# Kernel optimization log

Hardware: AMD Instinct MI355X
Metric: run time of the kernel (lower is better)

Reference implementation:

```python
import jax, jax.numpy as jnp
import numpy as np

FP8_MAX = 448.0   # e4m3 max finite value
BLOCK = 128


def _cast_e4m3(v):
    """Fake-cast to fp8 e4m3: round to nearest representable value (3 mantissa bits,
    min normal exponent -6, subnormal step 2^-9), saturate at +-448."""
    a = jnp.minimum(jnp.abs(v), FP8_MAX)
    e = jnp.floor(jnp.log2(jnp.maximum(a, jnp.float32(2.0) ** -9)))
    e = jnp.maximum(e, -6.0)                 # subnormal range
    step = jnp.exp2(e - 3.0)                 # 3 mantissa bits
    q = jnp.round(a / step) * step
    q = jnp.minimum(q, FP8_MAX)
    return jnp.sign(v) * q


def fake_quant_blockwise(x, br, bc):
    """Per-(br x bc)-tile scale = amax/448, cast to e4m3, dequantize."""
    R, C = x.shape
    xt = x.reshape(R // br, br, C // bc, bc)
    amax = jnp.max(jnp.abs(xt), axis=(1, 3), keepdims=True)
    scale = jnp.maximum(amax, 1e-12) / FP8_MAX
    q = _cast_e4m3(xt / scale) * scale
    return q.reshape(R, C)


def setup_inputs() -> dict:
    key = jax.random.key(0)
    k1, k2 = jax.random.split(key)
    x = jax.random.normal(k1, (8192, 4096), dtype=jnp.float32)
    weight = jax.random.normal(k2, (4096, 4096), dtype=jnp.float32) * 0.02
    bias = jnp.zeros((4096,), dtype=jnp.float32)
    return {"x": x, "weight": weight, "bias": bias}


def reference(x, weight, bias):
    # activations: per-row 1x128 blocks (is_left); weight: 128x128 square tiles (is_sqtile)
    x_fq = fake_quant_blockwise(x, 1, BLOCK)
    w_fq = fake_quant_blockwise(weight, BLOCK, BLOCK)
    return jnp.einsum('ti,oi->to', x_fq, w_fq) + bias
```

## Files before the change

kernel.cpp:

```cpp
#include <hip/hip_runtime.h>

#define M_DIM 8192
#define N_DIM 4096
#define K_DIM 4096

typedef __bf16 bf16x8 __attribute__((ext_vector_type(8)));
typedef float f32x4 __attribute__((ext_vector_type(4)));

__device__ __forceinline__ unsigned short f2bf(float f) {
    unsigned u = __float_as_uint(f);
    u += 0x7FFFu + ((u >> 16) & 1u);
    return (unsigned short)(u >> 16);
}

__device__ __forceinline__ float cast_e4m3(float v) {
    float a = fminf(fabsf(v), 448.0f);
    float am = fmaxf(a, 0x1p-9f);
    int e = (int)((__float_as_uint(am) >> 23) & 0xFFu) - 127;
    e = (e < -6) ? -6 : e;
    float step = __uint_as_float((unsigned)(e - 3 + 127) << 23);
    float q = rintf(a / step) * step;
    q = fminf(q, 448.0f);
    return (v < 0.0f) ? -q : q;
}

__global__ __launch_bounds__(256) void quant_x(const float* __restrict__ X,
                                               unsigned short* __restrict__ Xq) {
    const int g = threadIdx.x >> 5;
    const int l = threadIdx.x & 31;
    const long rb = (long)blockIdx.x * 8 + g;
    const int row = (int)(rb >> 5);
    const int kb = (int)(rb & 31);
    const size_t base = (size_t)row * K_DIM + kb * 128 + l * 4;
    const float4 v = *(const float4*)&X[base];
    float amax = fmaxf(fmaxf(fabsf(v.x), fabsf(v.y)), fmaxf(fabsf(v.z), fabsf(v.w)));
    #pragma unroll
    for (int m = 16; m >= 1; m >>= 1)
        amax = fmaxf(amax, __shfl_xor(amax, m));
    const float scale = fmaxf(amax, 1e-12f) / 448.0f;
    ushort4 o;
    o.x = f2bf(cast_e4m3(v.x / scale) * scale);
    o.y = f2bf(cast_e4m3(v.y / scale) * scale);
    o.z = f2bf(cast_e4m3(v.z / scale) * scale);
    o.w = f2bf(cast_e4m3(v.w / scale) * scale);
    *(ushort4*)&Xq[base] = o;
}

__global__ __launch_bounds__(256) void quant_w(const float* __restrict__ W,
                                               unsigned short* __restrict__ Wq) {
    const int tile = blockIdx.x;
    const int tr = tile >> 5;
    const int tc = tile & 31;
    const int t = threadIdx.x;
    const int c4 = (t & 31) * 4;
    const float* base = W + (size_t)(tr * 128) * K_DIM + tc * 128;

    float4 v[16];
    float amax = 0.0f;
    #pragma unroll
    for (int p = 0; p < 16; ++p) {
        const int r = p * 8 + (t >> 5);
        v[p] = *(const float4*)&base[(size_t)r * K_DIM + c4];
        amax = fmaxf(amax, fmaxf(fmaxf(fabsf(v[p].x), fabsf(v[p].y)),
                                 fmaxf(fabsf(v[p].z), fabsf(v[p].w))));
    }
    #pragma unroll
    for (int m = 32; m >= 1; m >>= 1)
        amax = fmaxf(amax, __shfl_xor(amax, m));
    __shared__ float red[4];
    if ((t & 63) == 0) red[t >> 6] = amax;
    __syncthreads();
    const float am4 = fmaxf(fmaxf(red[0], red[1]), fmaxf(red[2], red[3]));
    const float scale = fmaxf(am4, 1e-12f) / 448.0f;

    unsigned short* out = Wq + (size_t)(tr * 128) * K_DIM + tc * 128;
    #pragma unroll
    for (int p = 0; p < 16; ++p) {
        const int r = p * 8 + (t >> 5);
        ushort4 o;
        o.x = f2bf(cast_e4m3(v[p].x / scale) * scale);
        o.y = f2bf(cast_e4m3(v[p].y / scale) * scale);
        o.z = f2bf(cast_e4m3(v[p].z / scale) * scale);
        o.w = f2bf(cast_e4m3(v[p].w / scale) * scale);
        *(ushort4*)&out[(size_t)r * K_DIM + c4] = o;
    }
}

#define GLOAD16(g, l)                                                          \
    __builtin_amdgcn_global_load_lds(                                          \
        (const __attribute__((address_space(1))) void*)(g),                    \
        (__attribute__((address_space(3))) void*)(l), 16, 0, 0)


#define BARRIER() __builtin_amdgcn_s_barrier()
#define LGKM0() asm volatile("s_waitcnt lgkmcnt(0)" ::: "memory")
#define LGKM8() asm volatile("s_waitcnt lgkmcnt(8)" ::: "memory")
#define VM4()   asm volatile("s_waitcnt vmcnt(4)" ::: "memory")
#define VM0()   asm volatile("s_waitcnt vmcnt(0)" ::: "memory")

#define STAGE(G, grow0, kt, ebase, ht) do {                                    \
    const unsigned short* _s0 = (G) +                                          \
        (size_t)((grow0) + (ht) * 128 + w * 8 + sr) * K_DIM + (kt) * 64 + src_col; \
    const unsigned short* _s1 = _s0 + (size_t)64 * K_DIM;                      \
    char* _lb = (char*)lds + (ebase) * 2 + ((ht) * 128 + w * 8) * 128;         \
    GLOAD16(_s0, _lb);                                                         \
    GLOAD16(_s1, _lb + 8192);                                                  \
} while (0)

#define LDA(mh, ebase) do {                                                    \
    _Pragma("unroll") for (int _m = 0; _m < 4; ++_m) {                         \
        const int _row = wm * 128 + (mh) * 64 + _m * 16 + lr;                  \
        a[_m][0] = *(const bf16x8*)&lds[(ebase) + _row * 64 + ((0  + hk) ^ rsw)]; \
        a[_m][1] = *(const bf16x8*)&lds[(ebase) + _row * 64 + ((32 + hk) ^ rsw)]; \
    }                                                                          \
} while (0)

#define LDB(nh, dst, ebase) do {                                               \
    _Pragma("unroll") for (int _n = 0; _n < 2; ++_n) {                         \
        const int _row = wn * 64 + (nh) * 32 + _n * 16 + lr;                   \
        dst[_n][0] = *(const bf16x8*)&lds[(ebase) + _row * 64 + ((0  + hk) ^ rsw)]; \
        dst[_n][1] = *(const bf16x8*)&lds[(ebase) + _row * 64 + ((32 + hk) ^ rsw)]; \
    }                                                                          \
} while (0)

#define MMA(mh, nh, bb) do {                                                   \
    _Pragma("unroll") for (int _m = 0; _m < 4; ++_m)                           \
    _Pragma("unroll") for (int _n = 0; _n < 2; ++_n)                           \
    _Pragma("unroll") for (int _k = 0; _k < 2; ++_k)                           \
        acc[(mh) * 4 + _m][(nh) * 2 + _n] =                                    \
            __builtin_amdgcn_mfma_f32_16x16x32_bf16(                           \
                a[_m][_k], bb[_n][_k], acc[(mh) * 4 + _m][(nh) * 2 + _n], 0, 0, 0); \
} while (0)

__global__ __launch_bounds__(512, 2) void gemm256(const unsigned short* __restrict__ A,
                                                  const unsigned short* __restrict__ B,
                                                  const float* __restrict__ bias,
                                                  float* __restrict__ C) {
    __shared__ __align__(16) unsigned short lds[65536];

    const int t = threadIdx.x;
    const int lane = t & 63;
    const int w = t >> 6;
    const int wm = w >> 2, wn = w & 3;

    int bid = blockIdx.x;
    bid = (bid & 7) * 64 + (bid >> 3);
    const int bm = bid >> 4, bn = bid & 15;
    const size_t brow = (size_t)bm * 256, bcol = (size_t)bn * 256;

    const int sr = lane >> 3;
    const int src_col = (((lane & 7) ^ ((lane >> 3) & 7)) << 3);
    const int lr = lane & 15;
    const int hk = (lane >> 4) * 8;
    const int rsw = (lane & 7) << 3;

    f32x4 acc[8][4] = {};
    bf16x8 a[4][2], b0[2][2], b1[2][2];

    STAGE(A, brow, 0, 0, 0);     STAGE(A, brow, 0, 0, 1);
    STAGE(B, bcol, 0, 32768, 0); STAGE(B, bcol, 0, 32768, 1);
    STAGE(B, bcol, 1, 49152, 0); STAGE(B, bcol, 1, 49152, 1);
    VM4(); BARRIER();

    for (int u = 0; u < 62; u += 2) {
        LDA(0, 0); LDB(0, b0, 32768);
        STAGE(A, brow, u + 1, 16384, 0);
        LGKM8();
        BARRIER(); LGKM0();
        __builtin_amdgcn_s_setprio(1); MMA(0, 0, b0); __builtin_amdgcn_s_setprio(0);
        BARRIER();
        LDB(1, b1, 32768);
        STAGE(A, brow, u + 1, 16384, 1);
        BARRIER(); LGKM0();
        __builtin_amdgcn_s_setprio(1); MMA(0, 1, b1); __builtin_amdgcn_s_setprio(0);
        BARRIER();
        LDA(1, 0);
        STAGE(B, bcol, u + 2, 32768, 0);
        BARRIER(); LGKM0();
        __builtin_amdgcn_s_setprio(1); MMA(1, 1, b1); __builtin_amdgcn_s_setprio(0);
        BARRIER();
        STAGE(B, bcol, u + 2, 32768, 1);
        BARRIER();
        __builtin_amdgcn_s_setprio(1); MMA(1, 0, b0); __builtin_amdgcn_s_setprio(0);
        VM4();
        BARRIER();
        LDA(0, 16384); LDB(0, b0, 49152);
        STAGE(A, brow, u + 2, 0, 0);
        LGKM8();
        BARRIER(); LGKM0();
        __builtin_amdgcn_s_setprio(1); MMA(0, 0, b0); __builtin_amdgcn_s_setprio(0);
        BARRIER();
        LDB(1, b1, 49152);
        STAGE(A, brow, u + 2, 0, 1);
        BARRIER(); LGKM0();
        __builtin_amdgcn_s_setprio(1); MMA(0, 1, b1); __builtin_amdgcn_s_setprio(0);
        BARRIER();
        LDA(1, 16384);
        STAGE(B, bcol, u + 3, 49152, 0);
        BARRIER(); LGKM0();
        __builtin_amdgcn_s_setprio(1); MMA(1, 1, b1); __builtin_amdgcn_s_setprio(0);
        BARRIER();
        STAGE(B, bcol, u + 3, 49152, 1);
        BARRIER();
        __builtin_amdgcn_s_setprio(1); MMA(1, 0, b0); __builtin_amdgcn_s_setprio(0);
        VM4();
        BARRIER();
    }

    LDA(0, 0); LDB(0, b0, 32768);
    STAGE(A, brow, 63, 16384, 0);
    BARRIER(); LGKM0(); MMA(0, 0, b0); BARRIER();

    LDB(1, b1, 32768);
    STAGE(A, brow, 63, 16384, 1);
    BARRIER(); LGKM0(); MMA(0, 1, b1); BARRIER();

    LDA(1, 0);
    BARRIER(); LGKM0(); MMA(1, 1, b1); BARRIER();

    BARRIER(); MMA(1, 0, b0); VM0(); BARRIER();

    LDA(0, 16384); LDB(0, b0, 49152);
    BARRIER(); LGKM0(); MMA(0, 0, b0); BARRIER();

    LDB(1, b1, 49152);
    BARRIER(); LGKM0(); MMA(0, 1, b1); BARRIER();

    LDA(1, 16384);
    BARRIER(); LGKM0(); MMA(1, 1, b1); BARRIER();

    MMA(1, 0, b0);

    #pragma unroll
    for (int i = 0; i < 8; ++i) {
        const size_t row_base = brow + wm * 128 + i * 16 + (lane >> 4) * 4;
        #pragma unroll
        for (int j = 0; j < 4; ++j) {
            const size_t col = bcol + wn * 64 + j * 16 + lr;
            const float bv = bias[col];
            #pragma unroll
            for (int jj = 0; jj < 4; ++jj)
                C[(row_base + jj) * (size_t)N_DIM + col] = acc[i][j][jj] + bv;
        }
    }
}

extern "C" void kernel_launch(void* const* d_in, const int* in_sizes, int n_in,
                              void* d_out, int out_size, void* d_ws, size_t ws_size,
                              hipStream_t stream) {
    const float* x = (const float*)d_in[0];
    const float* w = (const float*)d_in[1];
    const float* bias = (const float*)d_in[2];
    float* out = (float*)d_out;

    unsigned short* xq = (unsigned short*)d_ws;
    unsigned short* wq = xq + (size_t)M_DIM * K_DIM;

    quant_x<<<(M_DIM * (K_DIM / 128)) / 8, 256, 0, stream>>>(x, xq);
    quant_w<<<(N_DIM / 128) * (K_DIM / 128), 256, 0, stream>>>(w, wq);
    gemm256<<<(M_DIM / 256) * (N_DIM / 256), 512, 0, stream>>>(xq, wq, bias, out);
}
```

Baseline: 292.1 us.

## Restructure GEMM main loop to prefetch deeper and drop the peeled epilogue

Reschedules the bf16 GEMM main loop so both B fragment halves are loaded from LDS up front. The A half-tile stage is issued one phase earlier, so vmcnt waits allow 6 outstanding global-to-LDS loads instead of 4. The loop now runs all 64 k-tiles, with STAGE clamping the k index to 63 so the trailing prefetches stay in bounds. This removes the separately peeled tail at the cost of a few redundant loads. Fewer LGKM waits come between MMA groups, aiming for more overlap of memory and MFMA work, but register pressure from holding b0 and b1 at once rises.

```diff
diff --git a/kernel.cpp b/kernel.cpp
--- a/kernel.cpp
+++ b/kernel.cpp
@@ -95,12 +95,13 @@
 #define BARRIER() __builtin_amdgcn_s_barrier()
 #define LGKM0() asm volatile("s_waitcnt lgkmcnt(0)" ::: "memory")
 #define LGKM8() asm volatile("s_waitcnt lgkmcnt(8)" ::: "memory")
-#define VM4()   asm volatile("s_waitcnt vmcnt(4)" ::: "memory")
+#define VM6()   asm volatile("s_waitcnt vmcnt(6)" ::: "memory")
 #define VM0()   asm volatile("s_waitcnt vmcnt(0)" ::: "memory")
 
 #define STAGE(G, grow0, kt, ebase, ht) do {                                    \
+    const int _kt = (kt) > 63 ? 63 : (kt);                                     \
     const unsigned short* _s0 = (G) +                                          \
-        (size_t)((grow0) + (ht) * 128 + w * 8 + sr) * K_DIM + (kt) * 64 + src_col; \
+        (size_t)((grow0) + (ht) * 128 + w * 8 + sr) * K_DIM + _kt * 64 + src_col; \
     const unsigned short* _s1 = _s0 + (size_t)64 * K_DIM;                      \
     char* _lb = (char*)lds + (ebase) * 2 + ((ht) * 128 + w * 8) * 128;         \
     GLOAD16(_s0, _lb);                                                         \
@@ -132,6 +133,9 @@
                 a[_m][_k], bb[_n][_k], acc[(mh) * 4 + _m][(nh) * 2 + _n], 0, 0, 0); \
 } while (0)
 
+#define PRIO1() __builtin_amdgcn_s_setprio(1)
+#define PRIO0() __builtin_amdgcn_s_setprio(0)
+
 __global__ __launch_bounds__(512, 2) void gemm256(const unsigned short* __restrict__ A,
                                                   const unsigned short* __restrict__ B,
                                                   const float* __restrict__ bias,
@@ -160,76 +164,53 @@
     STAGE(A, brow, 0, 0, 0);     STAGE(A, brow, 0, 0, 1);
     STAGE(B, bcol, 0, 32768, 0); STAGE(B, bcol, 0, 32768, 1);
     STAGE(B, bcol, 1, 49152, 0); STAGE(B, bcol, 1, 49152, 1);
-    VM4(); BARRIER();
-
-    for (int u = 0; u < 62; u += 2) {
-        LDA(0, 0); LDB(0, b0, 32768);
-        STAGE(A, brow, u + 1, 16384, 0);
+    STAGE(A, brow, 1, 16384, 0);
+    VM6(); BARRIER();
+
+    for (int u = 0; u < 64; u += 2) {
+        LDA(0, 0); LDB(0, b0, 32768); LDB(1, b1, 32768);
+        STAGE(A, brow, u + 1, 16384, 1);
         LGKM8();
         BARRIER(); LGKM0();
-        __builtin_amdgcn_s_setprio(1); MMA(0, 0, b0); __builtin_amdgcn_s_setprio(0);
-        BARRIER();
-        LDB(1, b1, 32768);
-        STAGE(A, brow, u + 1, 16384, 1);
-        BARRIER(); LGKM0();
-        __builtin_amdgcn_s_setprio(1); MMA(0, 1, b1); __builtin_amdgcn_s_setprio(0);
+        PRIO1(); MMA(0, 0, b0); PRIO0();
+        BARRIER();
+        STAGE(B, bcol, u + 2, 32768, 0);
+        BARRIER();
+        PRIO1(); MMA(0, 1, b1); PRIO0();
         BARRIER();
         LDA(1, 0);
-        STAGE(B, bcol, u + 2, 32768, 0);
-        BARRIER(); LGKM0();
-        __builtin_amdgcn_s_setprio(1); MMA(1, 1, b1); __builtin_amdgcn_s_setprio(0);
-        BARRIER();
         STAGE(B, bcol, u + 2, 32768, 1);
-        BARRIER();
-        __builtin_amdgcn_s_setprio(1); MMA(1, 0, b0); __builtin_amdgcn_s_setprio(0);
-        VM4();
-        BARRIER();
-        LDA(0, 16384); LDB(0, b0, 49152);
+        BARRIER(); LGKM0();
+        PRIO1(); MMA(1, 1, b1); PRIO0();
+        BARRIER();
         STAGE(A, brow, u + 2, 0, 0);
+        BARRIER();
+        PRIO1(); MMA(1, 0, b0); PRIO0();
+        VM6();
+        BARRIER();
+        LDA(0, 16384); LDB(0, b0, 49152); LDB(1, b1, 49152);
+        STAGE(A, brow, u + 2, 0, 1);
         LGKM8();
         BARRIER(); LGKM0();
-        __builtin_amdgcn_s_setprio(1); MMA(0, 0, b0); __builtin_amdgcn_s_setprio(0);
-        BARRIER();
-        LDB(1, b1, 49152);
-        STAGE(A, brow, u + 2, 0, 1);
-        BARRIER(); LGKM0();
-        __builtin_amdgcn_s_setprio(1); MMA(0, 1, b1); __builtin_amdgcn_s_setprio(0);
+        PRIO1(); MMA(0, 0, b0); PRIO0();
+        BARRIER();
+        STAGE(B, bcol, u + 3, 49152, 0);
+        BARRIER();
+        PRIO1(); MMA(0, 1, b1); PRIO0();
         BARRIER();
         LDA(1, 16384);
-        STAGE(B, bcol, u + 3, 49152, 0);
-        BARRIER(); LGKM0();
-        __builtin_amdgcn_s_setprio(1); MMA(1, 1, b1); __builtin_amdgcn_s_setprio(0);
-        BARRIER();
         STAGE(B, bcol, u + 3, 49152, 1);
-        BARRIER();
-        __builtin_amdgcn_s_setprio(1); MMA(1, 0, b0); __builtin_amdgcn_s_setprio(0);
-        VM4();
-        BARRIER();
-    }
-
-    LDA(0, 0); LDB(0, b0, 32768);
-    STAGE(A, brow, 63, 16384, 0);
-    BARRIER(); LGKM0(); MMA(0, 0, b0); BARRIER();
-
-    LDB(1, b1, 32768);
-    STAGE(A, brow, 63, 16384, 1);
-    BARRIER(); LGKM0(); MMA(0, 1, b1); BARRIER();
-
-    LDA(1, 0);
-    BARRIER(); LGKM0(); MMA(1, 1, b1); BARRIER();
-
-    BARRIER(); MMA(1, 0, b0); VM0(); BARRIER();
-
-    LDA(0, 16384); LDB(0, b0, 49152);
-    BARRIER(); LGKM0(); MMA(0, 0, b0); BARRIER();
-
-    LDB(1, b1, 49152);
-    BARRIER(); LGKM0(); MMA(0, 1, b1); BARRIER();
-
-    LDA(1, 16384);
-    BARRIER(); LGKM0(); MMA(1, 1, b1); BARRIER();
-
-    MMA(1, 0, b0);
+        BARRIER(); LGKM0();
+        PRIO1(); MMA(1, 1, b1); PRIO0();
+        BARRIER();
+        STAGE(A, brow, u + 3, 16384, 0);
+        BARRIER();
+        PRIO1(); MMA(1, 0, b0); PRIO0();
+        VM6();
+        BARRIER();
+    }
+
+    VM0();
 
     #pragma unroll
     for (int i = 0; i < 8; ++i) {
```

New measurement: 293.8 us. Within noise of the previous version (+0.6%).
